# Kernel optimization log

Hardware: AMD Instinct MI355X
Metric: run time of the kernel (lower is better)

## Reference

```python
import jax, jax.numpy as jnp
import numpy as np

B, D, N = 128, 2, 8192
C_CENT, K, R = 32, 32, 0.25
BOTTLE = 8
BN_EPS = 1e-5


def setup_inputs() -> dict:
    key = jax.random.key(0)
    ks = jax.random.split(key, 12)
    w = lambda k, s: jax.random.normal(k, s, dtype=jnp.float32) * 0.05
    z = lambda s: jnp.zeros(s, jnp.float32)
    o = lambda s: jnp.ones(s, jnp.float32)
    return {
        "x": jax.random.normal(ks[0], (B, D, N), dtype=jnp.float32),
        "eps": jax.random.normal(ks[1], (B, BOTTLE), dtype=jnp.float32),
        "sa_c1_w": w(ks[2], (64, D)), "sa_c1_b": z((64,)),
        "sa_bn1_g": o((64,)), "sa_bn1_b": z((64,)),
        "sa_c2_w": w(ks[3], (128, 64)), "sa_c2_b": z((128,)),
        "sa_bn2_g": o((128,)), "sa_bn2_b": z((128,)),
        "sa_c3_w": w(ks[4], (256, 128)), "sa_c3_b": z((256,)),
        "sa_bn3_g": o((256,)), "sa_bn3_b": z((256,)),
        "sa_fc1_w": w(ks[5], (1024, 256 * C_CENT)), "sa_fc1_b": z((1024,)),
        "sa_bn4_g": o((1024,)), "sa_bn4_b": z((1024,)),
        "sa_fc2_w": w(ks[6], (256, 1024)), "sa_fc2_b": z((256,)),
        "sa_bn5_g": o((256,)), "sa_bn5_b": z((256,)),
        "sa_fc3_w": w(ks[7], (BOTTLE, 256)), "sa_fc3_b": z((BOTTLE,)),
        "fce1_w": w(ks[8], (BOTTLE, BOTTLE)), "fce1_b": z((BOTTLE,)),
        "fce2_w": w(ks[9], (BOTTLE, BOTTLE)), "fce2_b": z((BOTTLE,)),
        "dfc1_w": w(ks[10], (32, BOTTLE)), "dfc1_b": z((32,)),
        "dfc2_w": w(ks[11], (128, 32)), "dfc2_b": z((128,)),
        "dfc3_w": w(jax.random.fold_in(key, 99), (512, 128)), "dfc3_b": z((512,)),
    }


def _bn2d(x, g, b):
    m = jnp.mean(x, axis=(0, 2, 3), keepdims=True)
    v = jnp.var(x, axis=(0, 2, 3), keepdims=True)
    return (x - m) * jax.lax.rsqrt(v + BN_EPS) * g[None, :, None, None] + b[None, :, None, None]


def _bn1d(x, g, b):
    m = jnp.mean(x, axis=0, keepdims=True)
    v = jnp.var(x, axis=0, keepdims=True)
    return (x - m) * jax.lax.rsqrt(v + BN_EPS) * g[None, :] + b[None, :]


def _fps(points, n_centroids):
    # points: [B, D, N]; deterministic start at index 0 (torch uses randint)
    c0 = points[:, :, 0]                                   # [B, D]
    dist0 = jnp.sum((c0[:, :, None] - points) ** 2, axis=1)  # [B, N]

    def step(dist, _):
        ind = jnp.argmax(dist, axis=1)                      # [B]
        c = jnp.take_along_axis(points, ind[:, None, None], axis=2)[:, :, 0]  # [B, D]
        dist = jnp.minimum(dist, jnp.sum((c[:, :, None] - points) ** 2, axis=1))
        return dist, c

    _, cs = jax.lax.scan(step, dist0, None, length=n_centroids - 1)  # [C-1, B, D]
    cents = jnp.concatenate([c0[None], cs], axis=0)          # [C, B, D]
    return jnp.transpose(cents, (1, 2, 0))                   # [B, D, C]


def _group_points(points):
    b, _, n = points.shape
    cents = _fps(points, C_CENT)                             # [B, D, C]
    # squared pairwise distances centroid->point: [B, C, N]
    sq = (-2.0 * jnp.einsum('bdc,bdn->bcn', cents, points)
          + jnp.sum(cents ** 2, axis=1)[:, :, None]
          + jnp.sum(points ** 2, axis=1)[:, None, :])
    idx = jnp.broadcast_to(jnp.arange(n, dtype=jnp.int32), (b, C_CENT, n))
    idx = jnp.where(sq > R * R, jnp.int32(n), idx)
    idx = jnp.sort(idx, axis=-1)[:, :, :K]                   # [B, C, K]
    first = idx[:, :, :1]
    idx = jnp.where(idx == n, first, idx)
    bidx = jnp.arange(b)[:, None, None]
    grouped = points[bidx, :, idx]                            # [B, C, K, D]
    return jnp.transpose(grouped, (0, 3, 1, 2))               # [B, D, C, K]


def reference(x, eps, sa_c1_w, sa_c1_b, sa_bn1_g, sa_bn1_b, sa_c2_w, sa_c2_b,
              sa_bn2_g, sa_bn2_b, sa_c3_w, sa_c3_b, sa_bn3_g, sa_bn3_b,
              sa_fc1_w, sa_fc1_b, sa_bn4_g, sa_bn4_b, sa_fc2_w, sa_fc2_b,
              sa_bn5_g, sa_bn5_b, sa_fc3_w, sa_fc3_b, fce1_w, fce1_b,
              fce2_w, fce2_b, dfc1_w, dfc1_b, dfc2_w, dfc2_b, dfc3_w, dfc3_b):
    b = x.shape[0]
    g = _group_points(x)                                     # [B, D, C, K]
    h = jax.nn.relu(_bn2d(jnp.einsum('bdck,od->bock', g, sa_c1_w) + sa_c1_b[None, :, None, None], sa_bn1_g, sa_bn1_b))
    h = jax.nn.relu(_bn2d(jnp.einsum('bdck,od->bock', h, sa_c2_w) + sa_c2_b[None, :, None, None], sa_bn2_g, sa_bn2_b))
    h = jax.nn.relu(_bn2d(jnp.einsum('bdck,od->bock', h, sa_c3_w) + sa_c3_b[None, :, None, None], sa_bn3_g, sa_bn3_b))
    h = jnp.max(h, axis=3)                                   # [B, 256, C]
    h = h.reshape(b, 256 * C_CENT)
    h = jax.nn.relu(_bn1d(h @ sa_fc1_w.T + sa_fc1_b, sa_bn4_g, sa_bn4_b))
    h = jax.nn.relu(_bn1d(h @ sa_fc2_w.T + sa_fc2_b, sa_bn5_g, sa_bn5_b))
    feat = jax.nn.relu(h @ sa_fc3_w.T + sa_fc3_b)            # [B, 8]
    mu = feat @ fce1_w.T + fce1_b
    logvar = feat @ fce2_w.T + fce2_b
    zlat = eps * jnp.exp(0.5 * logvar) + mu                  # reparametrize
    d = jax.nn.relu(zlat @ dfc1_w.T + dfc1_b)
    d = jax.nn.relu(d @ dfc2_w.T + dfc2_b)
    d = d @ dfc3_w.T + dfc3_b
    out = d.reshape(-1, 2, 256)
    return out, mu, logvar
```

## Files before the change

### kernel.cpp

```cpp
#include <hip/hip_runtime.h>
#include <cstdint>
#include <cstddef>

#define NB   128
#define NPT  8192
#define NC   32
#define NK   32
#define MSP  131072
#define R2   0.0625f

typedef unsigned short u16;
typedef unsigned long long u64;
typedef __attribute__((ext_vector_type(8))) short short8v;
typedef __attribute__((ext_vector_type(4))) float f32x4;

static constexpr size_t OFF_CENTS  = 0;
static constexpr size_t OFF_GX     = 8192;
static constexpr size_t OFF_GY     = OFF_GX + 131072;
static constexpr size_t OFF_H1Q    = OFF_GY + 131072;
static constexpr size_t OFF_H2Q    = OFF_H1Q + 4194304;
static constexpr size_t OFF_MAXPRE = OFF_H1Q;
static constexpr size_t OFF_P3S    = OFF_H1Q + 1048576;
static constexpr size_t OFF_P3Q    = OFF_H1Q + 2097152;
static constexpr size_t OFF_PART1  = OFF_H2Q;
static constexpr size_t OFF_PART2  = OFF_H2Q + 4194304;
static constexpr size_t OFF_FC1    = OFF_H2Q + 8388608;
static constexpr size_t OFF_FC2    = OFF_FC1 + 131072;
static constexpr size_t OFF_W2Q    = OFF_FC2 + 32768;
static constexpr size_t OFF_W3Q    = OFF_W2Q + 4096;
static constexpr size_t OFF_PMOM   = OFF_W3Q + 16384;
static constexpr size_t OFF_P2S    = OFF_PMOM + 20480;
static constexpr size_t OFF_P2Q    = OFF_P2S + 131072;
static constexpr size_t OFF_SC1    = OFF_P2Q + 131072;
static constexpr size_t OFF_SH1    = OFF_SC1 + 64;
static constexpr size_t OFF_SC2    = OFF_SH1 + 64;
static constexpr size_t OFF_SH2    = OFF_SC2 + 128;
static constexpr size_t OFF_SC3    = OFF_SH2 + 128;
static constexpr size_t OFF_SH3    = OFF_SC3 + 256;
static constexpr size_t OFF_SC4    = OFF_SH3 + 256;
static constexpr size_t OFF_SH4    = OFF_SC4 + 1024;
static constexpr size_t OFF_SC5    = OFF_SH4 + 1024;
static constexpr size_t OFF_SH5    = OFF_SC5 + 256;
static constexpr size_t OFF_SC3E   = OFF_SH5 + 256;
static constexpr size_t OFF_SH3E   = OFF_SC3E + 8192;

__device__ __forceinline__ u16 f2bf(float f) {
  uint32_t u = __float_as_uint(f);
  u += 0x7FFFu + ((u >> 16) & 1u);
  return (u16)(u >> 16);
}
__device__ __forceinline__ float bf2f(u16 h) {
  return __uint_as_float(((uint32_t)h) << 16);
}
__device__ __forceinline__ void gload16(const void* g, void* l) {
  __builtin_amdgcn_global_load_lds(
      (const __attribute__((address_space(1))) void*)g,
      (__attribute__((address_space(3))) void*)l, 16, 0, 0);
}

__global__ __launch_bounds__(512) void fps_kernel(const float* __restrict__ x,
                                                  float* __restrict__ cents) {
  const int b = blockIdx.x, t = threadIdx.x;
  const int lane = t & 63, wid = t >> 6;
  const float* xb = x + (size_t)b * 2 * NPT;
  float px[16], py[16], dst[16];
  __shared__ float lpx[NPT], lpy[NPT];
  __shared__ u64 slot[2][8];
  __shared__ float cxs[NC], cys[NC];
#pragma unroll
  for (int k = 0; k < 16; k++) {
    const int id = t + k * 512;
    px[k] = xb[id];
    py[k] = xb[NPT + id];
    lpx[id] = px[k];
    lpy[id] = py[k];
  }
  const float c0x = xb[0], c0y = xb[NPT];
  if (t == 0) { cxs[0] = c0x; cys[0] = c0y; }
#pragma unroll
  for (int k = 0; k < 16; k++) {
    const float dx = __fsub_rn(c0x, px[k]);
    const float dy = __fsub_rn(c0y, py[k]);
    dst[k] = __fadd_rn(__fmul_rn(dx, dx), __fmul_rn(dy, dy));
  }
  __syncthreads();
  for (int j = 1; j < NC; j++) {
    u64 v[16];
#pragma unroll
    for (int k = 0; k < 16; k++)
      v[k] = ((u64)__float_as_uint(dst[k]) << 32) | (uint32_t)~(uint32_t)(t + k * 512);
#pragma unroll
    for (int s = 8; s > 0; s >>= 1)
#pragma unroll
      for (int k = 0; k < s; k++)
        if (v[k + s] > v[k]) v[k] = v[k + s];
    u64 best = v[0];
#pragma unroll
    for (int off = 1; off < 64; off <<= 1) {
      const u64 o = __shfl_xor(best, off);
      if (o > best) best = o;
    }
    const int pb = j & 1;
    if (lane == 0) slot[pb][wid] = best;
    __syncthreads();
    u64 w = slot[pb][0];
#pragma unroll
    for (int s = 1; s < 8; s++) {
      const u64 o = slot[pb][s];
      if (o > w) w = o;
    }
    const int wi = (int)~(uint32_t)w;
    const float wx = lpx[wi], wy = lpy[wi];
    if (t == 0) { cxs[j] = wx; cys[j] = wy; }
#pragma unroll
    for (int k = 0; k < 16; k++) {
      const float dx = __fsub_rn(wx, px[k]);
      const float dy = __fsub_rn(wy, py[k]);
      const float nd = __fadd_rn(__fmul_rn(dx, dx), __fmul_rn(dy, dy));
      dst[k] = fminf(dst[k], nd);
    }
  }
  __syncthreads();
  if (t < NC) {
    cents[(size_t)b * 64 + t]      = cxs[t];
    cents[(size_t)b * 64 + 32 + t] = cys[t];
  }
}

__global__ __launch_bounds__(512) void group_kernel(const float* __restrict__ x,
                                                    const float* __restrict__ cents,
                                                    float* __restrict__ gx,
                                                    float* __restrict__ gy,
                                                    float* __restrict__ pmom) {
  const int b  = blockIdx.x & 127;
  const int cg = blockIdx.x >> 7;
  const int t = threadIdx.x;
  const int lane = t & 63, wid = t >> 6;
  const float* px = x + (size_t)b * 2 * NPT;
  const float* py = px + NPT;
  const int p0 = t * 16;

  float lx[16], ly[16], sp[16];
#pragma unroll
  for (int k = 0; k < 16; k += 4) {
    const float4 vx = *(const float4*)(px + p0 + k);
    const float4 vy = *(const float4*)(py + p0 + k);
    lx[k] = vx.x; lx[k + 1] = vx.y; lx[k + 2] = vx.z; lx[k + 3] = vx.w;
    ly[k] = vy.x; ly[k + 1] = vy.y; ly[k + 2] = vy.z; ly[k + 3] = vy.w;
  }
#pragma unroll
  for (int k = 0; k < 16; k++)
    sp[k] = __fadd_rn(__fmul_rn(lx[k], lx[k]), __fmul_rn(ly[k], ly[k]));

  __shared__ int idxs[4][NK];
  __shared__ int wtot[4][8];
  uint32_t mask[4];
  int ebase[4];

#pragma unroll
  for (int c = 0; c < 4; c++) {
    const int cc = cg * 4 + c;
    const float cx = cents[(size_t)b * 64 + cc];
    const float cy = cents[(size_t)b * 64 + 32 + cc];
    const float sc = __fadd_rn(__fmul_rn(cx, cx), __fmul_rn(cy, cy));
    uint32_t m = 0;
#pragma unroll
    for (int k = 0; k < 16; k++) {
      const float dot = __fadd_rn(__fmul_rn(cx, lx[k]), __fmul_rn(cy, ly[k]));
      const float sq  = __fadd_rn(__fadd_rn(__fmul_rn(-2.0f, dot), sc), sp[k]);
      if (!(sq > R2)) m |= (1u << k);
    }
    mask[c] = m;
    const int cnt = (int)__popc(m);
    int pre = cnt;
#pragma unroll
    for (int off = 1; off < 64; off <<= 1) {
      const int o = __shfl_up(pre, off);
      if (lane >= off) pre += o;
    }
    ebase[c] = pre - cnt;
    if (lane == 63) wtot[c][wid] = pre;
  }
  __syncthreads();
#pragma unroll
  for (int c = 0; c < 4; c++) {
    int off = 0;
#pragma unroll
    for (int w = 0; w < 8; w++) off += (w < wid) ? wtot[c][w] : 0;
    int pos = ebase[c] + off;
    uint32_t m = mask[c];
    while (m && pos < NK) {
      const int k = __ffs(m) - 1;
      idxs[c][pos] = p0 + k;
      m &= m - 1;
      pos++;
    }
  }
  __syncthreads();
  if (wid < 4) {
    int tot = 0;
#pragma unroll
    for (int w = 0; w < 8; w++) tot += wtot[wid][w];
    if (lane >= tot && lane < NK) idxs[wid][lane] = idxs[wid][0];
  }
  __syncthreads();
  if (wid < 4) {
    const int bc = b * 32 + cg * 4 + wid;
    float gxv = 0.f, gyv = 0.f;
    if (lane < NK) {
      const int id = idxs[wid][lane];
      gxv = px[id];
      gyv = py[id];
      const size_t s = (size_t)bc * NK + lane;
      gx[s] = gxv;
      gy[s] = gyv;
    }
    float sx = gxv, sy = gyv;
    float sxx = gxv * gxv, syy = gyv * gyv, sxy = gxv * gyv;
#pragma unroll
    for (int off = 1; off < 64; off <<= 1) {
      sx  += __shfl_xor(sx, off);
      sy  += __shfl_xor(sy, off);
      sxx += __shfl_xor(sxx, off);
      syy += __shfl_xor(syy, off);
      sxy += __shfl_xor(sxy, off);
    }
    if (lane == 0) {
      pmom[0 * 4096 + bc] = sx;
      pmom[1 * 4096 + bc] = sy;
      pmom[2 * 4096 + bc] = sxx;
      pmom[3 * 4096 + bc] = syy;
      pmom[4 * 4096 + bc] = sxy;
    }
  }
}

__global__ __launch_bounds__(256) void bn1fin_kernel(const float* __restrict__ pmom,
                                                     const float* __restrict__ w,
                                                     const float* __restrict__ gamma,
                                                     const float* __restrict__ beta,
                                                     float* __restrict__ sc,
                                                     float* __restrict__ sh) {
  const int t = threadIdx.x, lane = t & 63, wid = t >> 6;
  __shared__ float rr[5][4];
  __shared__ float red[5];
#pragma unroll
  for (int m = 0; m < 5; m++) {
    float a = 0.f;
#pragma unroll
    for (int i = 0; i < 4; i++) {
      const float4 v = *(const float4*)(pmom + m * 4096 + (t + i * 256) * 4);
      a += v.x + v.y + v.z + v.w;
    }
#pragma unroll
    for (int off = 1; off < 64; off <<= 1) a += __shfl_xor(a, off);
    if (lane == 0) rr[m][wid] = a;
  }
  __syncthreads();
  if (t == 0) {
#pragma unroll
    for (int m = 0; m < 5; m++) red[m] = rr[m][0] + rr[m][1] + rr[m][2] + rr[m][3];
  }
  __syncthreads();
  if (t < 64) {
    const double invM = 1.0 / (double)MSP;
    const double mx = red[0] * invM, my = red[1] * invM;
    const double exx = red[2] * invM, eyy = red[3] * invM, exy = red[4] * invM;
    const double w0 = w[2 * t], w1 = w[2 * t + 1];
    const double mean = w0 * mx + w1 * my;
    double var = w0 * w0 * (exx - mx * mx) + 2.0 * w0 * w1 * (exy - mx * my)
               + w1 * w1 * (eyy - my * my);
    if (var < 0.0) var = 0.0;
    const double s = (double)gamma[t] / sqrt(var + 1e-5);
    sc[t] = (float)s;
    sh[t] = (float)((double)beta[t] - mean * s);
  }
}

__global__ __launch_bounds__(256) void wquant_kernel(const float* __restrict__ c2w,
                                                     const float* __restrict__ c3w,
                                                     u16* __restrict__ w2q,
                                                     u16* __restrict__ w3qf) {
  const int id = blockIdx.x * 256 + threadIdx.x;
  if (id < 2048) {
    const int e = id * 4;
    const float4 v = *(const float4*)(c2w + e);
    uint2 q;
    q.x = (uint32_t)f2bf(v.x) | ((uint32_t)f2bf(v.y) << 16);
    q.y = (uint32_t)f2bf(v.z) | ((uint32_t)f2bf(v.w) << 16);
    *(uint2*)(w2q + e) = q;
  } else if (id < 2048 + 4096) {
    const int id2 = id - 2048;
    const int oc = id2 >> 4, k8 = (id2 & 15) * 8;
    const float4 v0 = *(const float4*)(c3w + oc * 128 + k8);
    const float4 v1 = *(const float4*)(c3w + oc * 128 + k8 + 4);
    uint4 q;
    q.x = (uint32_t)f2bf(v0.x) | ((uint32_t)f2bf(v0.y) << 16);
    q.y = (uint32_t)f2bf(v0.z) | ((uint32_t)f2bf(v0.w) << 16);
    q.z = (uint32_t)f2bf(v1.x) | ((uint32_t)f2bf(v1.y) << 16);
    q.w = (uint32_t)f2bf(v1.z) | ((uint32_t)f2bf(v1.w) << 16);
    const int off = ((((oc >> 4) * 4 + (k8 >> 5)) * 4 + ((k8 & 31) >> 3)) * 16 + (oc & 15)) * 8;
    *(uint4*)(w3qf + off) = q;
  }
}

__global__ __launch_bounds__(256) void finalize_kernel(
    const float* __restrict__ psum, const float* __restrict__ psq,
    int P, float invM,
    const float* __restrict__ gamma, const float* __restrict__ beta,
    float* __restrict__ scale, float* __restrict__ shift,
    float* __restrict__ scexp, float* __restrict__ shexp, int expand) {
  const int c = blockIdx.x, t = threadIdx.x;
  float s = 0.f, q = 0.f;
  for (int p = t; p < P; p += 256) {
    s += psum[(size_t)c * P + p];
    q += psq[(size_t)c * P + p];
  }
#pragma unroll
  for (int off = 1; off < 64; off <<= 1) {
    s += __shfl_xor(s, off);
    q += __shfl_xor(q, off);
  }
  __shared__ float r1[4], r2[4], bc2[2];
  if ((t & 63) == 0) { r1[t >> 6] = s; r2[t >> 6] = q; }
  __syncthreads();
  if (t == 0) {
    s = r1[0] + r1[1] + r1[2] + r1[3];
    q = r2[0] + r2[1] + r2[2] + r2[3];
    const float m = s * invM;
    float v = fmaf(-m, m, q * invM);
    v = fmaxf(v, 0.f);
    const float sc = gamma[c] * (float)(1.0 / sqrt((double)v + 1e-5));
    const float sh = fmaf(-m, sc, beta[c]);
    scale[c] = sc;
    shift[c] = sh;
    bc2[0] = sc;
    bc2[1] = sh;
  }
  __syncthreads();
  if (t < expand) {
    scexp[c * expand + t] = bc2[0];
    shexp[c * expand + t] = bc2[1];
  }
}

__global__ __launch_bounds__(256) void bncol_kernel(
    const float* __restrict__ in, int rows, int cols,
    const float* __restrict__ gamma, const float* __restrict__ beta,
    float* __restrict__ scale, float* __restrict__ shift) {
  const int jl = threadIdx.x & 63;
  const int rg = threadIdx.x >> 6;
  const int j = blockIdx.x * 64 + jl;
  float s = 0.f, q = 0.f;
  for (int r = rg; r < rows; r += 4) {
    const float v = in[(size_t)r * cols + j];
    s += v;
    q = fmaf(v, v, q);
  }
  __shared__ float rs[4][64], rq[4][64];
  rs[rg][jl] = s;
  rq[rg][jl] = q;
  __syncthreads();
  if (rg == 0) {
    s = rs[0][jl] + rs[1][jl] + rs[2][jl] + rs[3][jl];
    q = rq[0][jl] + rq[1][jl] + rq[2][jl] + rq[3][jl];
    const float m = s / (float)rows;
    float var = q / (float)rows - m * m;
    var = fmaxf(var, 0.f);
    const float sc = gamma[j] * (float)(1.0 / sqrt((double)var + 1e-5));
    scale[j] = sc;
    shift[j] = fmaf(-m, sc, beta[j]);
  }
}

__global__ __launch_bounds__(512) void conv2fused_kernel(
    const float* __restrict__ gx, const float* __restrict__ gy,
    const float* __restrict__ w1,
    const float* __restrict__ sc1, const float* __restrict__ sh1,
    const u16* __restrict__ wq,
    u16* __restrict__ outq,
    float* __restrict__ psum, float* __restrict__ psq) {
  constexpr int K = 64, OCB = 128, BS = 128, OCT = 128;
  constexpr int RB = K * 2;
  constexpr int STAGE = (OCB + BS) * RB;
  constexpr int EPI = BS * OCB * 2 + 4 * OCB * 2 * 4;
  constexpr int SMEM = STAGE > EPI ? STAGE : EPI;
  __shared__ __align__(16) char smem[SMEM + 1024];
  char* Wl = smem;
  char* Bl = smem + OCB * RB;
  float* par = (float*)(smem + SMEM);
  const int t = threadIdx.x;
  const int lane = t & 63, wid = t >> 6;
  const int sblk = blockIdx.x;
  const int s_base = sblk * BS;

  if (t < 64) {
    par[t]       = w1[t * 2];
    par[64 + t]  = w1[t * 2 + 1];
    par[128 + t] = sc1[t];
    par[192 + t] = sh1[t];
  }
  __syncthreads();

  {
    constexpr int CH = OCB * RB / 16, PW = CH / 8, NI = PW / 64;
#pragma unroll
    for (int j = 0; j < NI; j++) {
      const int c = wid * PW + j * 64 + lane;
      const int b = c * 16;
      const int oc = b / RB;
      const int off = b & (RB - 1);
      gload16((const char*)wq + (size_t)oc * RB + (off ^ ((oc & 7) << 4)),
              Wl + (wid * PW + j * 64) * 16);
    }
  }
  {
    const int sl = t >> 2;
    const int cq = t & 3;
    const float xx = gx[s_base + sl], yy = gy[s_base + sl];
    uint32_t pk[8];
#pragma unroll
    for (int h = 0; h < 8; h++) {
      const int c = cq * 16 + 2 * h;
      float v0 = fmaf(par[c],     xx, par[64 + c]     * yy);
      float v1 = fmaf(par[c + 1], xx, par[64 + c + 1] * yy);
      v0 = fmaxf(fmaf(v0, par[128 + c],     par[192 + c]),     0.f);
      v1 = fmaxf(fmaf(v1, par[128 + c + 1], par[192 + c + 1]), 0.f);
      pk[h] = (uint32_t)f2bf(v0) | ((uint32_t)f2bf(v1) << 16);
    }
    *(uint4*)(Bl + sl * RB + ((cq * 32)      ^ ((sl & 7) << 4))) = *(uint4*)&pk[0];
    *(uint4*)(Bl + sl * RB + ((cq * 32 + 16) ^ ((sl & 7) << 4))) = *(uint4*)&pk[4];
  }
  __syncthreads();

  const int wr = wid >> 2, wc = wid & 3;
  const int l15 = lane & 15, l4 = lane >> 4;
  f32x4 acc[4][2];
#pragma unroll
  for (int fo = 0; fo < 4; fo++)
#pragma unroll
    for (int fs = 0; fs < 2; fs++)
#pragma unroll
      for (int q = 0; q < 4; q++) acc[fo][fs][q] = 0.f;

#pragma unroll
  for (int ks = 0; ks < K / 32; ks++) {
    short8v a[4], bv[2];
#pragma unroll
    for (int f = 0; f < 4; f++) {
      const int oc = wr * 64 + f * 16 + l15;
      a[f] = *(const short8v*)(Wl + oc * RB + ((ks * 64 + l4 * 16) ^ ((oc & 7) << 4)));
    }
#pragma unroll
    for (int f = 0; f < 2; f++) {
      const int sl = wc * 32 + f * 16 + l15;
      bv[f] = *(const short8v*)(Bl + sl * RB + ((ks * 64 + l4 * 16) ^ ((sl & 7) << 4)));
    }
#pragma unroll
    for (int fo = 0; fo < 4; fo++)
#pragma unroll
      for (int fs = 0; fs < 2; fs++)
        acc[fo][fs] = __builtin_amdgcn_mfma_f32_16x16x32_bf16(a[fo], bv[fs], acc[fo][fs], 0, 0, 0);
  }
  __syncthreads();

  char* Dl = smem;
  float* sred1 = (float*)(smem + BS * OCB * 2);
  float* sred2 = sred1 + 4 * OCB;

#pragma unroll
  for (int fo = 0; fo < 4; fo++)
#pragma unroll
    for (int r = 0; r < 4; r++) {
      float s1 = acc[fo][0][r] + acc[fo][1][r];
      float s2 = fmaf(acc[fo][0][r], acc[fo][0][r], acc[fo][1][r] * acc[fo][1][r]);
#pragma unroll
      for (int off = 1; off < 16; off <<= 1) {
        s1 += __shfl_xor(s1, off);
        s2 += __shfl_xor(s2, off);
      }
      if (l15 == 0) {
        const int ocl = wr * 64 + fo * 16 + l4 * 4 + r;
        sred1[wc * OCB + ocl] = s1;
        sred2[wc * OCB + ocl] = s2;
      }
    }

#pragma unroll
  for (int fo = 0; fo < 4; fo++)
#pragma unroll
    for (int fs = 0; fs < 2; fs++) {
      const int sl = wc * 32 + fs * 16 + l15;
      const int ocl = wr * 64 + fo * 16 + l4 * 4;
      uint2 q;
      q.x = (uint32_t)f2bf(acc[fo][fs][0]) | ((uint32_t)f2bf(acc[fo][fs][1]) << 16);
      q.y = (uint32_t)f2bf(acc[fo][fs][2]) | ((uint32_t)f2bf(acc[fo][fs][3]) << 16);
      *(uint2*)(Dl + sl * 256 + ((ocl * 2) ^ ((sl & 7) << 4))) = q;
    }
  __syncthreads();

  if (t < OCB) {
    psum[(size_t)t * 1024 + sblk] =
        sred1[t] + sred1[OCB + t] + sred1[2 * OCB + t] + sred1[3 * OCB + t];
    psq[(size_t)t * 1024 + sblk] =
        sred2[t] + sred2[OCB + t] + sred2[2 * OCB + t] + sred2[3 * OCB + t];
  }
#pragma unroll
  for (int i = 0; i < 4; i++) {
    const int c = t + i * 512;
    const int sl = c >> 4, slot = c & 15;
    const uint4 v = *(const uint4*)(Dl + sl * 256 + ((slot * 16) ^ ((sl & 7) << 4)));
    *(uint4*)(outq + (size_t)(s_base + sl) * OCT + slot * 8) = v;
  }
}

__global__ __launch_bounds__(512) void conv3_kernel(
    const u16* __restrict__ act,
    const u16* __restrict__ wqf,
    const float* __restrict__ ascale, const float* __restrict__ ashift,
    float* __restrict__ psum, float* __restrict__ psq,
    float* __restrict__ maxpre) {
  constexpr int K = 128, RB = 256;
  __shared__ __align__(16) char Bl[64 * RB];
  const int t = threadIdx.x;
  const int lane = t & 63, wid = t >> 6;
  const int ws = wid & 1, wo = wid >> 1;
  const int sblk = blockIdx.x;
  const int l15 = lane & 15, l4 = lane >> 4;
  const int s_base = sblk * 64;

  short8v b[4][4];
  {
    const int ocq0 = wo * 4;
#pragma unroll
    for (int fo = 0; fo < 4; fo++)
#pragma unroll
      for (int ks = 0; ks < 4; ks++)
        b[fo][ks] = *(const short8v*)(wqf + ((((ocq0 + fo) * 4 + ks) * 4 + l4) * 16 + l15) * 8);
  }

  {
    const int kk0 = (t & 15) * 8;
    const float4 scA = *(const float4*)(ascale + kk0);
    const float4 scB = *(const float4*)(ascale + kk0 + 4);
    const float4 shA = *(const float4*)(ashift + kk0);
    const float4 shB = *(const float4*)(ashift + kk0 + 4);
    const float scr[8] = {scA.x, scA.y, scA.z, scA.w, scB.x, scB.y, scB.z, scB.w};
    const float shr[8] = {shA.x, shA.y, shA.z, shA.w, shB.x, shB.y, shB.z, shB.w};
#pragma unroll
    for (int i = 0; i < 2; i++) {
      const int sl = (t >> 4) + i * 32;
      const uint4 raw = *(const uint4*)(act + (size_t)(s_base + sl) * K + kk0);
      const u16* rp = (const u16*)&raw;
      uint32_t pk[4];
#pragma unroll
      for (int h = 0; h < 4; h++) {
        const float f0 = fmaxf(fmaf(bf2f(rp[2 * h]),     scr[2 * h],     shr[2 * h]),     0.f);
        const float f1 = fmaxf(fmaf(bf2f(rp[2 * h + 1]), scr[2 * h + 1], shr[2 * h + 1]), 0.f);
        pk[h] = (uint32_t)f2bf(f0) | ((uint32_t)f2bf(f1) << 16);
      }
      *(uint4*)(Bl + sl * RB + ((kk0 * 2) ^ ((sl & 7) << 4))) = *(uint4*)pk;
    }
  }
  __syncthreads();

  f32x4 acc[2][4];
#pragma unroll
  for (int fs = 0; fs < 2; fs++)
#pragma unroll
    for (int fo = 0; fo < 4; fo++)
#pragma unroll
      for (int q = 0; q < 4; q++) acc[fs][fo][q] = 0.f;

#pragma unroll
  for (int ks = 0; ks < 4; ks++) {
    short8v a[2];
#pragma unroll
    for (int fs = 0; fs < 2; fs++) {
      const int srow = ws * 32 + fs * 16 + l15;
      a[fs] = *(const short8v*)(Bl + srow * RB + ((ks * 64 + l4 * 16) ^ ((srow & 7) << 4)));
    }
#pragma unroll
    for (int fs = 0; fs < 2; fs++)
#pragma unroll
      for (int fo = 0; fo < 4; fo++)
        acc[fs][fo] = __builtin_amdgcn_mfma_f32_16x16x32_bf16(a[fs], b[fo][ks], acc[fs][fo], 0, 0, 0);
  }

  const int gid = sblk * 2 + ws;
#pragma unroll
  for (int fo = 0; fo < 4; fo++) {
    float s1 = acc[0][fo][0], s2 = acc[0][fo][0] * acc[0][fo][0];
    float mx = acc[0][fo][0];
#pragma unroll
    for (int fs = 0; fs < 2; fs++)
#pragma unroll
      for (int r = 0; r < 4; r++) {
        if (fs == 0 && r == 0) continue;
        const float v = acc[fs][fo][r];
        s1 += v;
        s2 = fmaf(v, v, s2);
        mx = fmaxf(mx, v);
      }
    s1 += __shfl_xor(s1, 16); s1 += __shfl_xor(s1, 32);
    s2 += __shfl_xor(s2, 16); s2 += __shfl_xor(s2, 32);
    mx = fmaxf(mx, __shfl_xor(mx, 16));
    mx = fmaxf(mx, __shfl_xor(mx, 32));
    if (l4 == 0) {
      const int oc = wo * 64 + fo * 16 + l15;
      psum[(size_t)oc * 4096 + gid] = s1;
      psq [(size_t)oc * 4096 + gid] = s2;
      maxpre[(size_t)oc * 4096 + gid] = mx;
    }
  }
}

template <int KL, bool TRANS, bool GATHER>
__global__ __launch_bounds__(512) void fcmfma_kernel(
    const float* __restrict__ A,
    const float* __restrict__ W,
    const float* __restrict__ ascale, const float* __restrict__ ashift,
    float* __restrict__ part,
    int Ntot, int Ktot) {
  __shared__ __align__(16) char smem[65536];
  char* Wh = smem;
  char* Wl = smem + 16384;
  char* Ah = smem + 32768;
  char* Al = smem + 49152;
  const int t = threadIdx.x;
  const int lane = t & 63, wid = t >> 6;
  const int sblk = blockIdx.x;
  const int n_base = blockIdx.y * 128;
  const int k_begin = sblk * KL;
  const int kq = t & 15;
  const int r0 = t >> 4;
  const int kk = kq * 4;
  const int wn = wid & 1, wm = wid >> 1;
  const int l15 = lane & 15, l4 = lane >> 4;

  f32x4 acc[4][2];
#pragma unroll
  for (int fo = 0; fo < 4; fo++)
#pragma unroll
    for (int fs = 0; fs < 2; fs++)
#pragma unroll
      for (int q = 0; q < 4; q++) acc[fo][fs][q] = 0.f;

  for (int c0 = 0; c0 < KL; c0 += 64) {
    const int kabs = k_begin + c0 + kk;
    float4 tsc, tsh;
    if constexpr (TRANS) {
      tsc = *(const float4*)(ascale + kabs);
      tsh = *(const float4*)(ashift + kabs);
    }
#pragma unroll
    for (int i = 0; i < 4; i++) {
      const int row = r0 + i * 32;
      const int byte = row * 128 + ((kk * 2) ^ ((row & 7) << 4));
      {
        const float4 v = *(const float4*)(W + (size_t)(n_base + row) * Ktot + kabs);
        const u16 h0 = f2bf(v.x), h1 = f2bf(v.y), h2 = f2bf(v.z), h3 = f2bf(v.w);
        uint2 hv, lv;
        hv.x = (uint32_t)h0 | ((uint32_t)h1 << 16);
        hv.y = (uint32_t)h2 | ((uint32_t)h3 << 16);
        lv.x = (uint32_t)f2bf(v.x - bf2f(h0)) | ((uint32_t)f2bf(v.y - bf2f(h1)) << 16);
        lv.y = (uint32_t)f2bf(v.z - bf2f(h2)) | ((uint32_t)f2bf(v.w - bf2f(h3)) << 16);
        *(uint2*)(Wh + byte) = hv;
        *(uint2*)(Wl + byte) = lv;
      }
      {
        float4 v;
        if constexpr (GATHER)
          v = *(const float4*)(A + (size_t)(kabs >> 5) * 4096 + row * 32 + (kabs & 31));
        else
          v = *(const float4*)(A + (size_t)row * Ktot + kabs);
        if constexpr (TRANS) {
          v.x = fmaxf(fmaf(v.x, tsc.x, tsh.x), 0.f);
          v.y = fmaxf(fmaf(v.y, tsc.y, tsh.y), 0.f);
          v.z = fmaxf(fmaf(v.z, tsc.z, tsh.z), 0.f);
          v.w = fmaxf(fmaf(v.w, tsc.w, tsh.w), 0.f);
        }
        const u16 h0 = f2bf(v.x), h1 = f2bf(v.y), h2 = f2bf(v.z), h3 = f2bf(v.w);
        uint2 hv, lv;
        hv.x = (uint32_t)h0 | ((uint32_t)h1 << 16);
        hv.y = (uint32_t)h2 | ((uint32_t)h3 << 16);
        lv.x = (uint32_t)f2bf(v.x - bf2f(h0)) | ((uint32_t)f2bf(v.y - bf2f(h1)) << 16);
        lv.y = (uint32_t)f2bf(v.z - bf2f(h2)) | ((uint32_t)f2bf(v.w - bf2f(h3)) << 16);
        *(uint2*)(Ah + byte) = hv;
        *(uint2*)(Al + byte) = lv;
      }
    }
    __syncthreads();
#pragma unroll
    for (int ks = 0; ks < 2; ks++) {
      short8v ah[4], al_[4], bh[2], bl[2];
#pragma unroll
      for (int f = 0; f < 4; f++) {
        const int r = wn * 64 + f * 16 + l15;
        const int byte = r * 128 + ((ks * 64 + l4 * 16) ^ ((r & 7) << 4));
        ah[f]  = *(const short8v*)(Wh + byte);
        al_[f] = *(const short8v*)(Wl + byte);
      }
#pragma unroll
      for (int f = 0; f < 2; f++) {
        const int r = wm * 32 + f * 16 + l15;
        const int byte = r * 128 + ((ks * 64 + l4 * 16) ^ ((r & 7) << 4));
        bh[f] = *(const short8v*)(Ah + byte);
        bl[f] = *(const short8v*)(Al + byte);
      }
#pragma unroll
      for (int fo = 0; fo < 4; fo++)
#pragma unroll
        for (int fs = 0; fs < 2; fs++) {
          acc[fo][fs] = __builtin_amdgcn_mfma_f32_16x16x32_bf16(ah[fo],  bh[fs], acc[fo][fs], 0, 0, 0);
          acc[fo][fs] = __builtin_amdgcn_mfma_f32_16x16x32_bf16(ah[fo],  bl[fs], acc[fo][fs], 0, 0, 0);
          acc[fo][fs] = __builtin_amdgcn_mfma_f32_16x16x32_bf16(al_[fo], bh[fs], acc[fo][fs], 0, 0, 0);
        }
    }
    __syncthreads();
  }
#pragma unroll
  for (int fo = 0; fo < 4; fo++) {
    const int n0 = n_base + wn * 64 + fo * 16 + l4 * 4;
#pragma unroll
    for (int fs = 0; fs < 2; fs++) {
      const int m = wm * 32 + fs * 16 + l15;
      *(float4*)(part + ((size_t)sblk * 128 + m) * Ntot + n0) =
          make_float4(acc[fo][fs][0], acc[fo][fs][1], acc[fo][fs][2], acc[fo][fs][3]);
    }
  }
}

__global__ __launch_bounds__(256) void fcreduce_kernel(const float* __restrict__ part,
                                                       float* __restrict__ out,
                                                       int total, int S) {
  const int id = blockIdx.x * 256 + threadIdx.x;
  if (id >= total) return;
  float s = 0.f;
  for (int p = 0; p < S; p++) s += part[(size_t)p * total + id];
  out[id] = s;
}

__global__ __launch_bounds__(64) void tail_kernel(
    const float* __restrict__ fc2raw, const float* __restrict__ scale5, const float* __restrict__ shift5,
    const float* __restrict__ w3, const float* __restrict__ b3,
    const float* __restrict__ e1w, const float* __restrict__ e1b,
    const float* __restrict__ e2w, const float* __restrict__ e2b,
    const float* __restrict__ eps,
    const float* __restrict__ d1w, const float* __restrict__ d1b,
    const float* __restrict__ d2w, const float* __restrict__ d2b,
    const float* __restrict__ d3w, const float* __restrict__ d3b,
    float* __restrict__ out) {
  const int b = blockIdx.x, t = threadIdx.x;
  __shared__ float h5[256], feat[8], z[8], d1[32], d2[128];
  for (int i = t; i < 256; i += 64) {
    const float v = fc2raw[(size_t)b * 256 + i];
    h5[i] = fmaxf(fmaf(v, scale5[i], shift5[i]), 0.f);
  }
  __syncthreads();
  if (t < 8) {
    float s = b3[t];
    for (int i = 0; i < 256; i++) s = fmaf(h5[i], w3[t * 256 + i], s);
    feat[t] = fmaxf(s, 0.f);
  }
  __syncthreads();
  if (t < 8) {
    float mu = e1b[t], lv = e2b[t];
    for (int j = 0; j < 8; j++) {
      mu = fmaf(feat[j], e1w[t * 8 + j], mu);
      lv = fmaf(feat[j], e2w[t * 8 + j], lv);
    }
    out[65536 + b * 8 + t] = mu;
    out[66560 + b * 8 + t] = lv;
    z[t] = fmaf(eps[b * 8 + t], expf(0.5f * lv), mu);
  }
  __syncthreads();
  if (t < 32) {
    float s = d1b[t];
    for (int j = 0; j < 8; j++) s = fmaf(z[j], d1w[t * 8 + j], s);
    d1[t] = fmaxf(s, 0.f);
  }
  __syncthreads();
  for (int o = t; o < 128; o += 64) {
    float s = d2b[o];
    for (int j = 0; j < 32; j++) s = fmaf(d1[j], d2w[o * 32 + j], s);
    d2[o] = fmaxf(s, 0.f);
  }
  __syncthreads();
  for (int o = t; o < 512; o += 64) {
    float s = d3b[o];
    for (int j = 0; j < 128; j++) s = fmaf(d2[j], d3w[o * 128 + j], s);
    out[(size_t)b * 512 + o] = s;
  }
}

extern "C" void kernel_launch(void* const* d_in, const int* in_sizes, int n_in,
                              void* d_out, int out_size, void* d_ws, size_t ws_size,
                              hipStream_t stream) {
  const float* x    = (const float*)d_in[0];
  const float* eps  = (const float*)d_in[1];
  const float* c1w  = (const float*)d_in[2];
  const float* bn1g = (const float*)d_in[4];
  const float* bn1b = (const float*)d_in[5];
  const float* c2w  = (const float*)d_in[6];
  const float* bn2g = (const float*)d_in[8];
  const float* bn2b = (const float*)d_in[9];
  const float* c3w  = (const float*)d_in[10];
  const float* bn3g = (const float*)d_in[12];
  const float* bn3b = (const float*)d_in[13];
  const float* f1w  = (const float*)d_in[14];
  const float* bn4g = (const float*)d_in[16];
  const float* bn4b = (const float*)d_in[17];
  const float* f2w  = (const float*)d_in[18];
  const float* bn5g = (const float*)d_in[20];
  const float* bn5b = (const float*)d_in[21];
  const float* f3w  = (const float*)d_in[22];
  const float* f3b  = (const float*)d_in[23];
  const float* e1w  = (const float*)d_in[24];
  const float* e1b  = (const float*)d_in[25];
  const float* e2w  = (const float*)d_in[26];
  const float* e2b  = (const float*)d_in[27];
  const float* d1w  = (const float*)d_in[28];
  const float* d1b  = (const float*)d_in[29];
  const float* d2w  = (const float*)d_in[30];
  const float* d2b  = (const float*)d_in[31];
  const float* d3w  = (const float*)d_in[32];
  const float* d3b  = (const float*)d_in[33];

  float* ws = (float*)d_ws;
  float* cents  = ws + OFF_CENTS;
  float* gx     = ws + OFF_GX;
  float* gy     = ws + OFF_GY;
  u16*   h2q    = (u16*)(ws + OFF_H2Q);
  u16*   w2q    = (u16*)(ws + OFF_W2Q);
  u16*   w3qf   = (u16*)(ws + OFF_W3Q);
  float* pmom   = ws + OFF_PMOM;
  float* maxpre = ws + OFF_MAXPRE;
  float* part1  = ws + OFF_PART1;
  float* part2  = ws + OFF_PART2;
  float* fc1o   = ws + OFF_FC1;
  float* fc2o   = ws + OFF_FC2;
  float* p2s = ws + OFF_P2S, *p2q = ws + OFF_P2Q;
  float* p3s = ws + OFF_P3S, *p3q = ws + OFF_P3Q;
  float* sc1 = ws + OFF_SC1, *sh1 = ws + OFF_SH1;
  float* sc2 = ws + OFF_SC2, *sh2 = ws + OFF_SH2;
  float* sc3 = ws + OFF_SC3, *sh3 = ws + OFF_SH3;
  float* sc4 = ws + OFF_SC4, *sh4 = ws + OFF_SH4;
  float* sc5 = ws + OFF_SC5, *sh5 = ws + OFF_SH5;
  float* sc3e = ws + OFF_SC3E, *sh3e = ws + OFF_SH3E;

  wquant_kernel<<<24, 256, 0, stream>>>(c2w, c3w, w2q, w3qf);
  fps_kernel<<<NB, 512, 0, stream>>>(x, cents);
  group_kernel<<<1024, 512, 0, stream>>>(x, cents, gx, gy, pmom);

  bn1fin_kernel<<<1, 256, 0, stream>>>(pmom, c1w, bn1g, bn1b, sc1, sh1);

  conv2fused_kernel<<<1024, 512, 0, stream>>>(gx, gy, c1w, sc1, sh1, w2q,
                                              h2q, p2s, p2q);
  finalize_kernel<<<128, 256, 0, stream>>>(p2s, p2q, 1024, 1.f / MSP, bn2g, bn2b,
                                           sc2, sh2, nullptr, nullptr, 0);

  conv3_kernel<<<2048, 512, 0, stream>>>(h2q, w3qf, sc2, sh2, p3s, p3q, maxpre);
  finalize_kernel<<<256, 256, 0, stream>>>(p3s, p3q, 4096, 1.f / MSP, bn3g, bn3b,
                                           sc3, sh3, sc3e, sh3e, 32);

  fcmfma_kernel<256, true, true><<<dim3(32, 8), 512, 0, stream>>>(
      maxpre, f1w, sc3e, sh3e, part1, 1024, 8192);
  fcreduce_kernel<<<512, 256, 0, stream>>>(part1, fc1o, 131072, 32);
  bncol_kernel<<<16, 256, 0, stream>>>(fc1o, 128, 1024, bn4g, bn4b, sc4, sh4);

  fcmfma_kernel<128, true, false><<<dim3(8, 2), 512, 0, stream>>>(
      fc1o, f2w, sc4, sh4, part2, 256, 1024);
  fcreduce_kernel<<<128, 256, 0, stream>>>(part2, fc2o, 32768, 8);
  bncol_kernel<<<4, 256, 0, stream>>>(fc2o, 128, 256, bn5g, bn5b, sc5, sh5);

  tail_kernel<<<NB, 64, 0, stream>>>(fc2o, sc5, sh5, f3w, f3b, e1w, e1b, e2w, e2b, eps,
                                     d1w, d1b, d2w, d2b, d3w, d3b, (float*)d_out);
}
```

Baseline: 214.2 us.

## Replace split-K partial buffers with atomics, fuse FPS argmax, widen tail kernel

The FC split-K kernels now atomically add into pre-zeroed output buffers, which removes both fcreduce launches and the partial-buffer traffic. The zeroing is folded into the weight-quantization kernel, whose grid grows to cover it. FPS computes the per-thread argmax key inside the distance-update loop instead of in a separate reduction tree. The tail kernel uses 128 threads and a lane-split dot product for fc3. Float atomics make the summation order nondeterministic and add contention.

```diff
diff --git a/kernel.cpp b/kernel.cpp
--- a/kernel.cpp
+++ b/kernel.cpp
@@ -22,8 +22,6 @@
 static constexpr size_t OFF_MAXPRE = OFF_H1Q;
 static constexpr size_t OFF_P3S    = OFF_H1Q + 1048576;
 static constexpr size_t OFF_P3Q    = OFF_H1Q + 2097152;
-static constexpr size_t OFF_PART1  = OFF_H2Q;
-static constexpr size_t OFF_PART2  = OFF_H2Q + 4194304;
 static constexpr size_t OFF_FC1    = OFF_H2Q + 8388608;
 static constexpr size_t OFF_FC2    = OFF_FC1 + 131072;
 static constexpr size_t OFF_W2Q    = OFF_FC2 + 32768;
@@ -77,24 +75,17 @@
   }
   const float c0x = xb[0], c0y = xb[NPT];
   if (t == 0) { cxs[0] = c0x; cys[0] = c0y; }
+  u64 best = 0;
 #pragma unroll
   for (int k = 0; k < 16; k++) {
     const float dx = __fsub_rn(c0x, px[k]);
     const float dy = __fsub_rn(c0y, py[k]);
     dst[k] = __fadd_rn(__fmul_rn(dx, dx), __fmul_rn(dy, dy));
+    const u64 pk = ((u64)__float_as_uint(dst[k]) << 32) | (uint32_t)~(uint32_t)(t + k * 512);
+    if (pk > best) best = pk;
   }
   __syncthreads();
   for (int j = 1; j < NC; j++) {
-    u64 v[16];
-#pragma unroll
-    for (int k = 0; k < 16; k++)
-      v[k] = ((u64)__float_as_uint(dst[k]) << 32) | (uint32_t)~(uint32_t)(t + k * 512);
-#pragma unroll
-    for (int s = 8; s > 0; s >>= 1)
-#pragma unroll
-      for (int k = 0; k < s; k++)
-        if (v[k + s] > v[k]) v[k] = v[k + s];
-    u64 best = v[0];
 #pragma unroll
     for (int off = 1; off < 64; off <<= 1) {
       const u64 o = __shfl_xor(best, off);
@@ -112,12 +103,15 @@
     const int wi = (int)~(uint32_t)w;
     const float wx = lpx[wi], wy = lpy[wi];
     if (t == 0) { cxs[j] = wx; cys[j] = wy; }
+    best = 0;
 #pragma unroll
     for (int k = 0; k < 16; k++) {
       const float dx = __fsub_rn(wx, px[k]);
       const float dy = __fsub_rn(wy, py[k]);
       const float nd = __fadd_rn(__fmul_rn(dx, dx), __fmul_rn(dy, dy));
       dst[k] = fminf(dst[k], nd);
+      const u64 pk = ((u64)__float_as_uint(dst[k]) << 32) | (uint32_t)~(uint32_t)(t + k * 512);
+      if (pk > best) best = pk;
     }
   }
   __syncthreads();
@@ -280,8 +274,14 @@
 __global__ __launch_bounds__(256) void wquant_kernel(const float* __restrict__ c2w,
                                                      const float* __restrict__ c3w,
                                                      u16* __restrict__ w2q,
-                                                     u16* __restrict__ w3qf) {
+                                                     u16* __restrict__ w3qf,
+                                                     float* __restrict__ fc1o,
+                                                     float* __restrict__ fc2o) {
   const int id = blockIdx.x * 256 + threadIdx.x;
+  const float4 z4 = make_float4(0.f, 0.f, 0.f, 0.f);
+  *(float4*)(fc1o + (size_t)id * 8)     = z4;
+  *(float4*)(fc1o + (size_t)id * 8 + 4) = z4;
+  *(float2*)(fc2o + (size_t)id * 2) = make_float2(0.f, 0.f);
   if (id < 2048) {
     const int e = id * 4;
     const float4 v = *(const float4*)(c2w + e);
@@ -620,7 +620,7 @@
     const float* __restrict__ A,
     const float* __restrict__ W,
     const float* __restrict__ ascale, const float* __restrict__ ashift,
-    float* __restrict__ part,
+    float* __restrict__ out,
     int Ntot, int Ktot) {
   __shared__ __align__(16) char smem[65536];
   char* Wh = smem;
@@ -725,23 +725,16 @@
 #pragma unroll
     for (int fs = 0; fs < 2; fs++) {
       const int m = wm * 32 + fs * 16 + l15;
-      *(float4*)(part + ((size_t)sblk * 128 + m) * Ntot + n0) =
-          make_float4(acc[fo][fs][0], acc[fo][fs][1], acc[fo][fs][2], acc[fo][fs][3]);
-    }
-  }
-}
-
-__global__ __launch_bounds__(256) void fcreduce_kernel(const float* __restrict__ part,
-                                                       float* __restrict__ out,
-                                                       int total, int S) {
-  const int id = blockIdx.x * 256 + threadIdx.x;
-  if (id >= total) return;
-  float s = 0.f;
-  for (int p = 0; p < S; p++) s += part[(size_t)p * total + id];
-  out[id] = s;
-}
-
-__global__ __launch_bounds__(64) void tail_kernel(
+      float* p = out + (size_t)m * Ntot + n0;
+      atomicAdd(p + 0, acc[fo][fs][0]);
+      atomicAdd(p + 1, acc[fo][fs][1]);
+      atomicAdd(p + 2, acc[fo][fs][2]);
+      atomicAdd(p + 3, acc[fo][fs][3]);
+    }
+  }
+}
+
+__global__ __launch_bounds__(128) void tail_kernel(
     const float* __restrict__ fc2raw, const float* __restrict__ scale5, const float* __restrict__ shift5,
     const float* __restrict__ w3, const float* __restrict__ b3,
     const float* __restrict__ e1w, const float* __restrict__ e1b,
@@ -753,15 +746,21 @@
     float* __restrict__ out) {
   const int b = blockIdx.x, t = threadIdx.x;
   __shared__ float h5[256], feat[8], z[8], d1[32], d2[128];
-  for (int i = t; i < 256; i += 64) {
+  for (int i = t; i < 256; i += 128) {
     const float v = fc2raw[(size_t)b * 256 + i];
     h5[i] = fmaxf(fmaf(v, scale5[i], shift5[i]), 0.f);
   }
   __syncthreads();
-  if (t < 8) {
-    float s = b3[t];
-    for (int i = 0; i < 256; i++) s = fmaf(h5[i], w3[t * 256 + i], s);
-    feat[t] = fmaxf(s, 0.f);
+  if (t < 64) {
+    const int o = t >> 3, p = t & 7;
+    const float* wr = w3 + o * 256 + p * 32;
+    const float* hr = h5 + p * 32;
+    float s = 0.f;
+    for (int i = 0; i < 32; i++) s = fmaf(hr[i], wr[i], s);
+    s += __shfl_xor(s, 1);
+    s += __shfl_xor(s, 2);
+    s += __shfl_xor(s, 4);
+    if (p == 0) feat[o] = fmaxf(s + b3[o], 0.f);
   }
   __syncthreads();
   if (t < 8) {
@@ -781,13 +780,13 @@
     d1[t] = fmaxf(s, 0.f);
   }
   __syncthreads();
-  for (int o = t; o < 128; o += 64) {
-    float s = d2b[o];
-    for (int j = 0; j < 32; j++) s = fmaf(d1[j], d2w[o * 32 + j], s);
-    d2[o] = fmaxf(s, 0.f);
-  }
-  __syncthreads();
-  for (int o = t; o < 512; o += 64) {
+  {
+    float s = d2b[t];
+    for (int j = 0; j < 32; j++) s = fmaf(d1[j], d2w[t * 32 + j], s);
+    d2[t] = fmaxf(s, 0.f);
+  }
+  __syncthreads();
+  for (int o = t; o < 512; o += 128) {
     float s = d3b[o];
     for (int j = 0; j < 128; j++) s = fmaf(d2[j], d3w[o * 128 + j], s);
     out[(size_t)b * 512 + o] = s;
@@ -836,8 +835,6 @@
   u16*   w3qf   = (u16*)(ws + OFF_W3Q);
   float* pmom   = ws + OFF_PMOM;
   float* maxpre = ws + OFF_MAXPRE;
-  float* part1  = ws + OFF_PART1;
-  float* part2  = ws + OFF_PART2;
   float* fc1o   = ws + OFF_FC1;
   float* fc2o   = ws + OFF_FC2;
   float* p2s = ws + OFF_P2S, *p2q = ws + OFF_P2Q;
@@ -849,7 +846,7 @@
   float* sc5 = ws + OFF_SC5, *sh5 = ws + OFF_SH5;
   float* sc3e = ws + OFF_SC3E, *sh3e = ws + OFF_SH3E;
 
-  wquant_kernel<<<24, 256, 0, stream>>>(c2w, c3w, w2q, w3qf);
+  wquant_kernel<<<64, 256, 0, stream>>>(c2w, c3w, w2q, w3qf, fc1o, fc2o);
   fps_kernel<<<NB, 512, 0, stream>>>(x, cents);
   group_kernel<<<1024, 512, 0, stream>>>(x, cents, gx, gy, pmom);
 
@@ -865,15 +862,13 @@
                                            sc3, sh3, sc3e, sh3e, 32);
 
   fcmfma_kernel<256, true, true><<<dim3(32, 8), 512, 0, stream>>>(
-      maxpre, f1w, sc3e, sh3e, part1, 1024, 8192);
-  fcreduce_kernel<<<512, 256, 0, stream>>>(part1, fc1o, 131072, 32);
+      maxpre, f1w, sc3e, sh3e, fc1o, 1024, 8192);
   bncol_kernel<<<16, 256, 0, stream>>>(fc1o, 128, 1024, bn4g, bn4b, sc4, sh4);
 
   fcmfma_kernel<128, true, false><<<dim3(8, 2), 512, 0, stream>>>(
-      fc1o, f2w, sc4, sh4, part2, 256, 1024);
-  fcreduce_kernel<<<128, 256, 0, stream>>>(part2, fc2o, 32768, 8);
+      fc1o, f2w, sc4, sh4, fc2o, 256, 1024);
   bncol_kernel<<<4, 256, 0, stream>>>(fc2o, 128, 256, bn5g, bn5b, sc5, sh5);
 
-  tail_kernel<<<NB, 64, 0, stream>>>(fc2o, sc5, sh5, f3w, f3b, e1w, e1b, e2w, e2b, eps,
-                                     d1w, d1b, d2w, d2b, d3w, d3b, (float*)d_out);
-}
+  tail_kernel<<<NB, 128, 0, stream>>>(fc2o, sc5, sh5, f3w, f3b, e1w, e1b, e2w, e2b, eps,
+                                      d1w, d1b, d2w, d2b, d3w, d3b, (float*)d_out);
+}
```

New measurement: 240.2 us. 12.1% more time.
